# Performance work log

Hardware: AMD Instinct MI355X
Metric: run time of the kernel (lower is better)

Reference implementation:

```python
import jax, jax.numpy as jnp
import numpy as np

N = 512          # nodes per sample (num_nodes)
B = 8            # batch size (samples)
H = 64           # hidden_dim
SPARSITY = 0.1
K = int(SPARSITY * N * (N - 1))  # edges kept per sample (fixed, static)


def setup_inputs() -> dict:
    key = jax.random.key(0)
    ks = jax.random.split(key, 8)

    def lin(k, fi, fo):
        w = jax.random.normal(k, (fi, fo), jnp.float32) / np.sqrt(fi).astype(np.float32)
        b = jnp.zeros((fo,), jnp.float32)
        return w, b

    w_emb, b_emb = lin(ks[0], 1, H)
    w_proj, b_proj = lin(ks[1], H, H)
    w1, b1 = lin(ks[2], 2 * H, H)
    w2, b2 = lin(ks[3], H, H // 2)
    w3, b3 = lin(ks[4], H // 2, 1)
    x = jax.random.uniform(ks[5], (B * N, 1), jnp.float32)  # abundances >= 0
    batch = jnp.repeat(jnp.arange(B, dtype=jnp.int32), N)   # [B*N]
    return dict(x=x, w_emb=w_emb, b_emb=b_emb, w_proj=w_proj, b_proj=b_proj,
                w1=w1, b1=b1, w2=w2, b2=b2, w3=w3, b3=b3, batch=batch)


def reference(x, w_emb, b_emb, w_proj, b_proj, w1, b1, w2, b2, w3, b3, batch):
    # node embedding + projection (dropout is eval-mode no-op)
    emb = jax.nn.relu(x @ w_emb + b_emb) @ w_proj + b_proj     # [B*N, H]
    emb = emb.reshape(B, N, H)
    # first pairwise-MLP layer: cat([e_i, e_j]) @ w1 == e_i @ w1a + e_j @ w1b
    w1a, w1b = w1[:H], w1[H:]
    ai = emb @ w1a                                            # [B, N, H]
    aj = emb @ w1b                                            # [B, N, H]
    h1 = jax.nn.relu(ai[:, :, None, :] + aj[:, None, :, :] + b1)   # [B, N, N, H]
    h2 = jax.nn.relu(jnp.einsum('bijh,hk->bijk', h1, w2) + b2)     # [B, N, N, H/2]
    probs = jax.nn.sigmoid(jnp.einsum('bijk,ko->bij', h2, w3) + b3[0])  # [B, N, N]
    probs = 0.5 * (probs + jnp.swapaxes(probs, 1, 2))          # symmetrize
    probs = probs * (1.0 - jnp.eye(N, dtype=probs.dtype))      # mask diagonal
    flat = probs.reshape(B, N * N)
    _, idx = jax.lax.top_k(flat, K)                            # [B, K]
    idx = jnp.sort(idx, axis=-1)                               # row-major order (dense_to_sparse)
    vals = jnp.take_along_axis(flat, idx, axis=-1)             # [B, K]
    offsets = (jnp.arange(B) * N)[:, None]                     # node offset per sample
    rows = idx // N + offsets
    cols = idx % N + offsets
    edge_index = jnp.stack([rows.reshape(-1), cols.reshape(-1)], axis=0)  # [2, B*K]
    edge_weights = vals.reshape(-1)                            # [B*K]
    adj = jnp.zeros((B, N * N), flat.dtype).at[jnp.arange(B)[:, None], idx].set(vals)
    adj = adj.reshape(B, N, N)                                 # sparse adjacency per sample
    return edge_index, edge_weights, adj
```

## Files before the change

kernel.cpp:

```cpp
#include <hip/hip_runtime.h>

#define NV 512
#define BV 8
#define KSEL 26163
#define NNv (NV*NV)
#define BKv (BV*KSEL)
#define CAPB 32768
#define DELTA 1e-4f

typedef unsigned int u32;
typedef __attribute__((ext_vector_type(2))) float f32x2;
typedef __attribute__((ext_vector_type(4))) float f32x4;
typedef __attribute__((ext_vector_type(4))) u32 u32x4;
typedef __attribute__((ext_vector_type(8))) _Float16 f16x8;

__device__ __forceinline__ f32x2 pk_add(f32x2 a, f32x2 b) {
    f32x2 d; asm("v_pk_add_f32 %0, %1, %2" : "=v"(d) : "v"(a), "v"(b)); return d;
}
__device__ __forceinline__ f32x2 pk_fma(f32x2 a, f32x2 b, f32x2 c) {
    f32x2 d; asm("v_pk_fma_f32 %0, %1, %2, %3" : "=v"(d) : "v"(a), "v"(b), "v"(c)); return d;
}
__device__ __forceinline__ u32 pkrtz(float a, float b) {
    u32 d; asm("v_cvt_pkrtz_f16_f32 %0, %1, %2" : "=v"(d) : "v"(a), "v"(b)); return d;
}
__device__ __forceinline__ float fast_sigmoid(float z) {
    float e, p;
    asm("v_exp_f32 %0, %1" : "=v"(e) : "v"(-z * 1.44269504f));
    asm("v_rcp_f32 %0, %1" : "=v"(p) : "v"(1.f + e));
    return p;
}

__global__ void __launch_bounds__(256) k_embed(
    const float* __restrict__ x, const float* __restrict__ w_emb,
    const float* __restrict__ b_emb, const float* __restrict__ w_proj,
    const float* __restrict__ b_proj, const float* __restrict__ w1,
    const float* __restrict__ b1,
    float* __restrict__ ai, float* __restrict__ aj,
    float* __restrict__ ai256, float* __restrict__ ajb256) {
    __shared__ float sh[4][64];
    __shared__ float se[4][64];
    const int c = threadIdx.x;
    const int lr = threadIdx.y;
    const int row = blockIdx.x * 4 + lr;
    const float xv = x[row];
    sh[lr][c] = fmaxf(fmaf(xv, w_emb[c], b_emb[c]), 0.f);
    __syncthreads();
    float e = 0.f;
#pragma unroll
    for (int h = 0; h < 64; ++h) e = fmaf(sh[lr][h], w_proj[h * 64 + c], e);
    se[lr][c] = e + b_proj[c];
    __syncthreads();
    float a0 = 0.f, a1 = 0.f;
#pragma unroll
    for (int h = 0; h < 64; ++h) {
        const float ev = se[lr][h];
        a0 = fmaf(ev, w1[h * 64 + c], a0);
        a1 = fmaf(ev, w1[(64 + h) * 64 + c], a1);
    }
    ai[row * 64 + c] = a0;
    aj[row * 64 + c] = a1;
    ai256[row * 64 + c] = a0 * 256.0f;
    ajb256[row * 64 + c] = (a1 + b1[c]) * 256.0f;
}

__global__ void __launch_bounds__(256) k_pairs_sym(
    const float* __restrict__ ai256, const float* __restrict__ ajb256,
    const float* __restrict__ w2, const float* __restrict__ b2,
    const float* __restrict__ w3, const float* __restrict__ b3,
    float* __restrict__ probs, u32* __restrict__ hist8) {
    __shared__ float sI[2048];
    __shared__ float sJ[2048];
    __shared__ float sp1[32 * 33];
    __shared__ float sp2[32 * 33];
    __shared__ u32 lh[1024];
    const int tid = threadIdx.x;
    const int b = blockIdx.y;
    int remb = blockIdx.x, ta = 0;
    while (remb >= 16 - ta) { remb -= 16 - ta; ++ta; }
    const int tb = ta + remb;
    const int i0 = ta << 5, j0 = tb << 5;
    {
        const int r = tid >> 3, c8v = (tid & 7) << 3;
        const float* srcI = &ai256[(((b << 9) + i0 + r) << 6) + c8v];
        *(float4*)&sI[(r << 6) + c8v]     = *(const float4*)&srcI[0];
        *(float4*)&sI[(r << 6) + c8v + 4] = *(const float4*)&srcI[4];
        const float* srcJ = &ai256[(((b << 9) + j0 + r) << 6) + c8v];
        *(float4*)&sJ[(r << 6) + c8v]     = *(const float4*)&srcJ[0];
        *(float4*)&sJ[(r << 6) + c8v + 4] = *(const float4*)&srcJ[4];
        lh[tid] = 0; lh[256 + tid] = 0; lh[512 + tid] = 0; lh[768 + tid] = 0;
    }
    const int lane = tid & 63;
    const int lp = lane & 15, lg = lane >> 4;
    const int wave = tid >> 6;
    const int dir = wave >> 1, wc = wave & 1;
    const int colb = (wc << 4) + lp;
    const int colg = (dir ? i0 : j0) + colb;

    alignas(16) float ajr[2][8];
    {
        const float* base = &ajb256[(((b << 9) + colg) << 6) + (lg << 3)];
        *(float4*)&ajr[0][0] = *(const float4*)&base[0];
        *(float4*)&ajr[0][4] = *(const float4*)&base[4];
        *(float4*)&ajr[1][0] = *(const float4*)&base[32];
        *(float4*)&ajr[1][4] = *(const float4*)&base[36];
    }
    f16x8 Ah[2][2], Al[2][2];
#pragma unroll
    for (int kt = 0; kt < 2; ++kt)
#pragma unroll
        for (int ch = 0; ch < 2; ++ch)
#pragma unroll
            for (int e = 0; e < 8; ++e) {
                const float wv2 = w2[((ch << 5) + (lg << 3) + e) * 32 + (kt << 4) + lp];
                const _Float16 wh = (_Float16)wv2;
                Ah[kt][ch][e] = wh;
                Al[kt][ch][e] = (_Float16)((wv2 - (float)wh) * 2048.0f);
            }
    float b2f[2][4], w3f[2][4];
#pragma unroll
    for (int kt = 0; kt < 2; ++kt)
#pragma unroll
        for (int r = 0; r < 4; ++r) {
            b2f[kt][r] = b2[(kt << 4) + (lg << 2) + r] * 256.0f;
            w3f[kt][r] = w3[(kt << 4) + (lg << 2) + r] * 0.00390625f;
        }
    const float b3v = b3[0];
    __syncthreads();

    const float* __restrict__ sA = dir ? sJ : sI;
    float* __restrict__ spO = dir ? sp2 : sp1;
    const f32x2 CN1 = {-1.f, -1.f};

    for (int r = 0; r < 32; ++r) {
        alignas(16) float ar[2][8];
        *(float4*)&ar[0][0] = *(const float4*)&sA[(r << 6) + (lg << 3)];
        *(float4*)&ar[0][4] = *(const float4*)&sA[(r << 6) + (lg << 3) + 4];
        *(float4*)&ar[1][0] = *(const float4*)&sA[(r << 6) + 32 + (lg << 3)];
        *(float4*)&ar[1][4] = *(const float4*)&sA[(r << 6) + 32 + (lg << 3) + 4];
        alignas(16) u32 hw[2][4], lw[2][4];
#pragma unroll
        for (int c = 0; c < 2; ++c)
#pragma unroll
            for (int e2 = 0; e2 < 4; ++e2) {
                const f32x2 a2 = *(const f32x2*)&ar[c][e2 * 2];
                const f32x2 j2 = *(const f32x2*)&ajr[c][e2 * 2];
                f32x2 u2 = pk_add(a2, j2);
                u2[0] = fmaxf(u2[0], 0.f);
                u2[1] = fmaxf(u2[1], 0.f);
                hw[c][e2] = pkrtz(u2[0], u2[1]);
                f32x2 hif;
                hif[0] = __uint_as_float(__float_as_uint(u2[0]) & 0xFFFFE000u);
                hif[1] = __uint_as_float(__float_as_uint(u2[1]) & 0xFFFFE000u);
                const f32x2 lo = pk_fma(hif, CN1, u2);
                lw[c][e2] = pkrtz(lo[0], lo[1]);
            }
        const f16x8 Bh0 = __builtin_bit_cast(f16x8, *(u32x4*)&hw[0][0]);
        const f16x8 Bh1 = __builtin_bit_cast(f16x8, *(u32x4*)&hw[1][0]);
        const f16x8 Bl0 = __builtin_bit_cast(f16x8, *(u32x4*)&lw[0][0]);
        const f16x8 Bl1 = __builtin_bit_cast(f16x8, *(u32x4*)&lw[1][0]);
        f32x4 am0 = {0.f,0.f,0.f,0.f}, am1 = {0.f,0.f,0.f,0.f};
        f32x4 ac0 = {0.f,0.f,0.f,0.f}, ac1 = {0.f,0.f,0.f,0.f};
        am0 = __builtin_amdgcn_mfma_f32_16x16x32_f16(Ah[0][0], Bh0, am0, 0, 0, 0);
        am0 = __builtin_amdgcn_mfma_f32_16x16x32_f16(Ah[0][1], Bh1, am0, 0, 0, 0);
        am0 = __builtin_amdgcn_mfma_f32_16x16x32_f16(Ah[0][0], Bl0, am0, 0, 0, 0);
        am0 = __builtin_amdgcn_mfma_f32_16x16x32_f16(Ah[0][1], Bl1, am0, 0, 0, 0);
        ac0 = __builtin_amdgcn_mfma_f32_16x16x32_f16(Al[0][0], Bh0, ac0, 0, 0, 0);
        ac0 = __builtin_amdgcn_mfma_f32_16x16x32_f16(Al[0][1], Bh1, ac0, 0, 0, 0);
        am1 = __builtin_amdgcn_mfma_f32_16x16x32_f16(Ah[1][0], Bh0, am1, 0, 0, 0);
        am1 = __builtin_amdgcn_mfma_f32_16x16x32_f16(Ah[1][1], Bh1, am1, 0, 0, 0);
        am1 = __builtin_amdgcn_mfma_f32_16x16x32_f16(Ah[1][0], Bl0, am1, 0, 0, 0);
        am1 = __builtin_amdgcn_mfma_f32_16x16x32_f16(Ah[1][1], Bl1, am1, 0, 0, 0);
        ac1 = __builtin_amdgcn_mfma_f32_16x16x32_f16(Al[1][0], Bh0, ac1, 0, 0, 0);
        ac1 = __builtin_amdgcn_mfma_f32_16x16x32_f16(Al[1][1], Bh1, ac1, 0, 0, 0);
        float s = 0.f;
#pragma unroll
        for (int q = 0; q < 4; ++q) {
            const float amc = fmaf(ac0[q], 4.8828125e-4f, am0[q]);
            s = fmaf(fmaxf(amc + b2f[0][q], 0.f), w3f[0][q], s);
        }
#pragma unroll
        for (int q = 0; q < 4; ++q) {
            const float amc = fmaf(ac1[q], 4.8828125e-4f, am1[q]);
            s = fmaf(fmaxf(amc + b2f[1][q], 0.f), w3f[1][q], s);
        }
        s += __shfl_xor(s, 16);
        s += __shfl_xor(s, 32);
        const float p = fast_sigmoid(s + b3v);
        if (lane < 16) {
            if (dir == 0) spO[r * 33 + colb] = p;
            else          spO[colb * 33 + r] = p;
        }
    }
    __syncthreads();

    {
        const int pr = tid >> 3;
        const int pc = (tid & 7) << 2;
        const int rep = (tid & 3) << 8;
        const bool diag = (ta == tb);
        float4 vo;
        float vq[4];
#pragma unroll
        for (int q = 0; q < 4; ++q) {
            float v = 0.5f * (sp1[pr * 33 + pc + q] + sp2[pr * 33 + pc + q]);
            if (diag && pr == pc + q) v = 0.f;
            vq[q] = v;
            atomicAdd(&lh[rep + (__float_as_uint(v) >> 24)], diag ? 1u : 2u);
        }
        vo.x = vq[0]; vo.y = vq[1]; vo.z = vq[2]; vo.w = vq[3];
        *(float4*)&probs[(((b << 9) + i0 + pr) << 9) + j0 + pc] = vo;
        if (!diag) {
            float4 w4;
            w4.x = 0.5f * (sp1[(pc + 0) * 33 + pr] + sp2[(pc + 0) * 33 + pr]);
            w4.y = 0.5f * (sp1[(pc + 1) * 33 + pr] + sp2[(pc + 1) * 33 + pr]);
            w4.z = 0.5f * (sp1[(pc + 2) * 33 + pr] + sp2[(pc + 2) * 33 + pr]);
            w4.w = 0.5f * (sp1[(pc + 3) * 33 + pr] + sp2[(pc + 3) * 33 + pr]);
            *(float4*)&probs[(((b << 9) + j0 + pr) << 9) + i0 + pc] = w4;
        }
    }
    __syncthreads();
    const u32 sum = lh[tid] + lh[256 + tid] + lh[512 + tid] + lh[768 + tid];
    if (sum) atomicAdd(&hist8[b * 256 + tid], sum);
}

__global__ void __launch_bounds__(256) k_hist13(
    const float* __restrict__ probs, const u32* __restrict__ hist8,
    u32* __restrict__ hist13) {
    __shared__ u32 lh[8192];
    __shared__ u32 s8[256];
    __shared__ u32 selsh;
    const int t = threadIdx.x;
    const int b = blockIdx.y;
    for (int k = t; k < 8192; k += 256) lh[k] = 0u;
    s8[t] = hist8[b * 256 + t];
    __syncthreads();
    for (int off = 1; off < 256; off <<= 1) {
        const u32 v = (t + off < 256) ? s8[t + off] : 0u;
        __syncthreads();
        s8[t] += v;
        __syncthreads();
    }
    {
        const u32 above = (t < 255) ? s8[t + 1] : 0u;
        if (s8[t] >= (u32)KSEL && above < (u32)KSEL) selsh = (u32)t;
    }
    __syncthreads();
    const u32 sel = selsh;
    const float* Pb = probs + b * NNv;
    const int base = blockIdx.x * 4096 + t;
#pragma unroll
    for (int e = 0; e < 16; ++e) {
        const u32 key = __float_as_uint(Pb[base + e * 256]);
        if ((key >> 24) == sel) atomicAdd(&lh[(key >> 11) & 8191u], 1u);
    }
    __syncthreads();
    for (int k = t; k < 8192; k += 256) {
        const u32 v = lh[k];
        if (v) atomicAdd(&hist13[b * 8192 + k], v);
    }
}

__global__ void __launch_bounds__(256) k_sel13(
    const u32* __restrict__ hist8, const u32* __restrict__ hist13,
    float* __restrict__ thr) {
    __shared__ u32 s8[256];
    __shared__ u32 s[256];
    __shared__ u32 c8sh, remsh;
    const int b = blockIdx.x, t = threadIdx.x;
    s8[t] = hist8[b * 256 + t];
    __syncthreads();
    for (int off = 1; off < 256; off <<= 1) {
        const u32 v = (t + off < 256) ? s8[t + off] : 0u;
        __syncthreads();
        s8[t] += v;
        __syncthreads();
    }
    {
        const u32 above = (t < 255) ? s8[t + 1] : 0u;
        if (s8[t] >= (u32)KSEL && above < (u32)KSEL) {
            c8sh = (u32)t;
            remsh = (u32)KSEL - above;
        }
    }
    __syncthreads();
    const u32 c8 = c8sh, remv = remsh;
    const u32* H = hist13 + b * 8192;
    u32 sum = 0;
    for (int k = 0; k < 32; ++k) sum += H[t * 32 + k];
    s[t] = sum;
    __syncthreads();
    for (int off = 1; off < 256; off <<= 1) {
        const u32 v = (t + off < 256) ? s[t + off] : 0u;
        __syncthreads();
        s[t] += v;
        __syncthreads();
    }
    const u32 above = (t < 255) ? s[t + 1] : 0u;
    if (s[t] >= remv && above < remv) {
        u32 cum = above;
        int c = 31;
        for (; c >= 0; --c) {
            cum += H[t * 32 + c];
            if (cum >= remv) break;
        }
        const u32 p21 = (c8 << 13) | (u32)(t * 32 + c);
        thr[b]     = __uint_as_float(p21 << 11) - 2.f * DELTA;
        thr[8 + b] = __uint_as_float((p21 + 1u) << 11) + 2.f * DELTA;
    }
}

__device__ __forceinline__ float exact_p(const float* __restrict__ rai,
                                         const float* __restrict__ raj,
                                         const float* __restrict__ s_w2,
                                         const float* __restrict__ s_b1,
                                         const float* __restrict__ s_b2,
                                         const float* __restrict__ s_w3,
                                         float b3v) {
    float acc[32];
#pragma unroll
    for (int k = 0; k < 32; ++k) acc[k] = 0.f;
#pragma unroll 1
    for (int h0 = 0; h0 < 64; h0 += 16) {
        float A[16], J[16];
#pragma unroll
        for (int q = 0; q < 4; ++q) {
            *(float4*)&A[q * 4] = *(const float4*)&rai[h0 + q * 4];
            *(float4*)&J[q * 4] = *(const float4*)&raj[h0 + q * 4];
        }
#pragma unroll
        for (int hh = 0; hh < 16; ++hh) {
            const float tv = fmaxf((A[hh] + J[hh]) + s_b1[h0 + hh], 0.f);
#pragma unroll
            for (int k = 0; k < 32; ++k) acc[k] = fmaf(tv, s_w2[(h0 + hh) * 32 + k], acc[k]);
        }
    }
    float d = 0.f;
#pragma unroll
    for (int k = 0; k < 32; ++k) d = fmaf(fmaxf(acc[k] + s_b2[k], 0.f), s_w3[k], d);
    return 1.f / (1.f + expf(-(d + b3v)));
}

__global__ void __launch_bounds__(256) k_band(
    const float* __restrict__ P, const float* __restrict__ thr,
    const float* __restrict__ ai, const float* __restrict__ aj,
    const float* __restrict__ b1, const float* __restrict__ w2,
    const float* __restrict__ b2, const float* __restrict__ w3,
    const float* __restrict__ b3,
    u32* __restrict__ C_in, u32* __restrict__ bandCnt,
    u32* __restrict__ bandIdx, float* __restrict__ bandVal,
    u32* __restrict__ bgt) {
    __shared__ float s_w2[2048];
    __shared__ float s_b1[64], s_b2[32], s_w3[32];
    __shared__ u32 lidx[2048];
    __shared__ u32 lcnt, lhi, gbase;
    const int b = blockIdx.y, blk = blockIdx.x, t = threadIdx.x;
    {
        const int o = t * 8;
        *(float4*)&s_w2[o]     = *(const float4*)&w2[o];
        *(float4*)&s_w2[o + 4] = *(const float4*)&w2[o + 4];
        if (t < 64) s_b1[t] = b1[t];
        if (t < 32) { s_b2[t] = b2[t]; s_w3[t] = w3[t]; }
        if (t == 0) { lcnt = 0u; lhi = 0u; }
    }
    __syncthreads();
    const float Tlo = thr[b], Thi = thr[8 + b];
    const int fi0 = blk * 1024 + t * 4;
    const float4 v = *(const float4*)&P[b * NNv + fi0];
    const float vv[4] = {v.x, v.y, v.z, v.w};
    u32 hc = 0;
#pragma unroll
    for (int q = 0; q < 4; ++q) {
        const float xq = vv[q];
        if (xq > Thi) ++hc;
        else if (xq >= Tlo) {
            const u32 p = atomicAdd(&lcnt, 1u);
            if (p < 2048u) lidx[p] = (u32)(fi0 + q);
        }
    }
    if (hc) atomicAdd(&lhi, hc);
    __syncthreads();
    if (t == 0) {
        bgt[b * 256 + blk] = lhi;
        if (lhi) atomicAdd(&C_in[b], lhi);
        gbase = lcnt ? atomicAdd(&bandCnt[b], lcnt) : 0u;
    }
    __syncthreads();
    const u32 ln = min(lcnt, 2048u);
    const float b3v = b3[0];
    for (u32 p = t; p < ln; p += 256) {
        const u32 g = gbase + p;
        if (g < (u32)CAPB) {
            const u32 idx = lidx[p];
            const int i = (int)(idx >> 9), j = (int)(idx & 511u);
            const float* ri  = &ai[(((b << 9) + i)) << 6];
            const float* rj  = &aj[(((b << 9) + j)) << 6];
            const float* rj2 = &ai[(((b << 9) + j)) << 6];
            const float* ri2 = &aj[(((b << 9) + i)) << 6];
            const float p1 = exact_p(ri, rj, s_w2, s_b1, s_b2, s_w3, b3v);
            const float p2 = exact_p(rj2, ri2, s_w2, s_b1, s_b2, s_w3, b3v);
            bandIdx[b * CAPB + g] = idx;
            bandVal[b * CAPB + g] = 0.5f * (p1 + p2);
        }
    }
}

__global__ void __launch_bounds__(256) k_band_select(
    const u32* __restrict__ bandCnt, const u32* __restrict__ C_in,
    const u32* __restrict__ bandIdx, const float* __restrict__ bandVal,
    u32* __restrict__ bitmap, const u32* __restrict__ bgt,
    u32* __restrict__ goff) {
    __shared__ u32 red[256];
    __shared__ u32 lsel[256];
    __shared__ u32 tie[8192];
    __shared__ u32 tieCnt;
    const int b = blockIdx.x, t = threadIdx.x;
    const u32 nb = min(bandCnt[b], (u32)CAPB);
    const u32 Kp = (u32)KSEL - C_in[b];
    const u32* vb = (const u32*)(bandVal + b * CAPB);
    const u32* ib = bandIdx + b * CAPB;
    u32* bm = bitmap + b * 8192;
    lsel[t] = 0u;
    u32 mn = 0xFFFFFFFFu, mx = 0u;
    for (u32 k = t; k < nb; k += 256) { const u32 v = vb[k]; mn = min(mn, v); mx = max(mx, v); }
    red[t] = mn; __syncthreads();
    for (int s = 128; s > 0; s >>= 1) { if (t < s) red[t] = min(red[t], red[t + s]); __syncthreads(); }
    const u32 glo = red[0]; __syncthreads();
    red[t] = mx; __syncthreads();
    for (int s = 128; s > 0; s >>= 1) { if (t < s) red[t] = max(red[t], red[t + s]); __syncthreads(); }
    const u32 ghi = red[0]; __syncthreads();
    u32 lo = glo, hi = ghi;
    while (lo < hi) {
        const u32 mid = lo + ((hi - lo) >> 1);
        u32 c = 0;
        for (u32 k = t; k < nb; k += 256) c += (vb[k] > mid);
        red[t] = c; __syncthreads();
        for (int s = 128; s > 0; s >>= 1) { if (t < s) red[t] += red[t + s]; __syncthreads(); }
        const u32 tot = red[0]; __syncthreads();
        if (tot >= Kp) lo = mid + 1; else hi = mid;
    }
    const u32 Tx = lo;
    if (t == 0) tieCnt = 0u;
    __syncthreads();
    u32 c = 0;
    for (u32 k = t; k < nb; k += 256) {
        const u32 v = vb[k];
        if (v > Tx) {
            ++c;
            const u32 idx = ib[k];
            atomicOr(&bm[idx >> 5], 1u << (idx & 31u));
            atomicAdd(&lsel[idx >> 10], 1u);
        } else if (v == Tx) {
            const u32 p = atomicAdd(&tieCnt, 1u);
            if (p < 8192u) tie[p] = ib[k];
        }
    }
    red[t] = c; __syncthreads();
    for (int s = 128; s > 0; s >>= 1) { if (t < s) red[t] += red[t + s]; __syncthreads(); }
    const u32 Ap = red[0]; __syncthreads();
    const u32 Rp = Kp - Ap;
    const u32 E = min(tieCnt, 8192u);
    for (u32 k = t; k < E; k += 256) {
        const u32 my = tie[k];
        u32 r = 0;
        for (u32 m = 0; m < E; ++m) r += (tie[m] < my);
        if (r < Rp) {
            atomicOr(&bm[my >> 5], 1u << (my & 31u));
            atomicAdd(&lsel[my >> 10], 1u);
        }
    }
    __syncthreads();
    const u32 g = bgt[b * 256 + t] + lsel[t];
    red[t] = g;
    __syncthreads();
    for (int off = 1; off < 256; off <<= 1) {
        const u32 a = (t >= off) ? red[t - off] : 0u;
        __syncthreads();
        red[t] += a;
        __syncthreads();
    }
    goff[b * 256 + t] = red[t] - g;
}

__global__ void k_write(const float* __restrict__ P, const float* __restrict__ thr,
                        const u32* __restrict__ bitmap, const u32* __restrict__ goff,
                        float* __restrict__ out) {
    __shared__ u32 sg[256];
    const int b = blockIdx.y, blk = blockIdx.x, t = threadIdx.x;
    const float Thi = thr[8 + b];
    const int pbase = b * NNv;
    const int fi0 = blk * 1024 + t * 4;
    const float4 v = *(const float4*)&P[pbase + fi0];
    const float vv[4] = {v.x, v.y, v.z, v.w};
    const u32 w = bitmap[b * 8192 + (fi0 >> 5)];
    const u32 sh = (u32)(fi0 & 31);
    bool sel[4];
    u32 cnt = 0;
#pragma unroll
    for (int q = 0; q < 4; ++q) {
        sel[q] = (vv[q] > Thi) || ((w >> (sh + q)) & 1u);
        cnt += sel[q];
    }
    sg[t] = cnt;
    __syncthreads();
    for (int off = 1; off < 256; off <<= 1) {
        const u32 a = (t >= off) ? sg[t - off] : 0u;
        __syncthreads();
        sg[t] += a;
        __syncthreads();
    }
    u32 pos = goff[b * 256 + blk] + sg[t] - cnt;
#pragma unroll
    for (int q = 0; q < 4; ++q) {
        if (sel[q]) {
            if (pos < (u32)KSEL) {
                const int g = b * KSEL + (int)pos;
                const int fi = fi0 + q;
                const int row = fi >> 9, col = fi & 511;
                out[g]           = (float)(row + (b << 9));
                out[BKv + g]     = (float)(col + (b << 9));
                out[2 * BKv + g] = vv[q];
                out[3 * BKv + pbase + fi] = vv[q];
            }
            ++pos;
        }
    }
}

extern "C" void kernel_launch(void* const* d_in, const int* in_sizes, int n_in,
                              void* d_out, int out_size, void* d_ws, size_t ws_size,
                              hipStream_t stream) {
    const float* x      = (const float*)d_in[0];
    const float* w_emb  = (const float*)d_in[1];
    const float* b_emb  = (const float*)d_in[2];
    const float* w_proj = (const float*)d_in[3];
    const float* b_proj = (const float*)d_in[4];
    const float* w1     = (const float*)d_in[5];
    const float* b1     = (const float*)d_in[6];
    const float* w2     = (const float*)d_in[7];
    const float* b2     = (const float*)d_in[8];
    const float* w3     = (const float*)d_in[9];
    const float* b3     = (const float*)d_in[10];
    (void)in_sizes; (void)n_in; (void)ws_size;

    char* ws = (char*)d_ws;
    float* ai      = (float*)(ws);
    float* aj      = (float*)(ws + 1048576);
    float* ai256   = (float*)(ws + 2097152);
    float* ajb256  = (float*)(ws + 3145728);
    float* probs   = (float*)(ws + 4194304);
    u32*   bandIdx = (u32*)  (ws + 12582912);
    float* bandVal = (float*)(ws + 13631488);
    const size_t SOFF = 14680064;
    u32*   hist8   = (u32*)  (ws + SOFF);
    u32*   hist13  = (u32*)  (ws + SOFF + 8192);
    float* thr     = (float*)(ws + SOFF + 270336);
    u32*   C_in    = (u32*)  (ws + SOFF + 270400);
    u32*   bandCnt = (u32*)  (ws + SOFF + 270432);
    u32*   bitmap  = (u32*)  (ws + SOFF + 270464);
    u32*   bgt     = (u32*)  (ws + SOFF + 532608);
    u32*   goff    = (u32*)  (ws + SOFF + 540800);

    float* out = (float*)d_out;

    hipMemsetAsync(d_out, 0, (size_t)out_size * sizeof(float), stream);
    hipMemsetAsync(ws + SOFF, 0, 532608, stream);

    k_embed<<<1024, dim3(64, 4, 1), 0, stream>>>(x, w_emb, b_emb, w_proj, b_proj,
                                                 w1, b1, ai, aj, ai256, ajb256);
    k_pairs_sym<<<dim3(136, 8), 256, 0, stream>>>(ai256, ajb256, w2, b2, w3, b3,
                                                  probs, hist8);
    k_hist13<<<dim3(64, 8), 256, 0, stream>>>(probs, hist8, hist13);
    k_sel13<<<8, 256, 0, stream>>>(hist8, hist13, thr);
    k_band<<<dim3(256, 8), 256, 0, stream>>>(probs, thr, ai, aj, b1, w2, b2, w3, b3,
                                             C_in, bandCnt, bandIdx, bandVal, bgt);
    k_band_select<<<8, 256, 0, stream>>>(bandCnt, C_in, bandIdx, bandVal,
                                         bitmap, bgt, goff);
    k_write<<<dim3(256, 8), 256, 0, stream>>>(probs, thr, bitmap, goff, out);
}
```

Measured before the change: 198.5 us.

## Split band exact recompute into separate load-balanced kernel; vectorize hist13 loads

```diff
diff --git a/kernel.cpp b/kernel.cpp
--- a/kernel.cpp
+++ b/kernel.cpp
@@ -247,11 +247,16 @@
     __syncthreads();
     const u32 sel = selsh;
     const float* Pb = probs + b * NNv;
-    const int base = blockIdx.x * 4096 + t;
-#pragma unroll
-    for (int e = 0; e < 16; ++e) {
-        const u32 key = __float_as_uint(Pb[base + e * 256]);
-        if ((key >> 24) == sel) atomicAdd(&lh[(key >> 11) & 8191u], 1u);
+    const int base = blockIdx.x * 4096 + t * 4;
+#pragma unroll
+    for (int e = 0; e < 4; ++e) {
+        const float4 v4 = *(const float4*)&Pb[base + e * 1024];
+        const float vv[4] = {v4.x, v4.y, v4.z, v4.w};
+#pragma unroll
+        for (int q = 0; q < 4; ++q) {
+            const u32 key = __float_as_uint(vv[q]);
+            if ((key >> 24) == sel) atomicAdd(&lh[(key >> 11) & 8191u], 1u);
+        }
     }
     __syncthreads();
     for (int k = t; k < 8192; k += 256) {
@@ -309,6 +314,44 @@
     }
 }
 
+__global__ void __launch_bounds__(256) k_band(
+    const float* __restrict__ P, const float* __restrict__ thr,
+    u32* __restrict__ C_in, u32* __restrict__ bandCnt, u32* __restrict__ bandIdx,
+    u32* __restrict__ bgt) {
+    __shared__ u32 lidx[2048];
+    __shared__ u32 lcnt, lhi, gbase;
+    const int b = blockIdx.y, blk = blockIdx.x, t = threadIdx.x;
+    if (t == 0) { lcnt = 0u; lhi = 0u; }
+    __syncthreads();
+    const float Tlo = thr[b], Thi = thr[8 + b];
+    const int fi0 = blk * 1024 + t * 4;
+    const float4 v = *(const float4*)&P[b * NNv + fi0];
+    const float vv[4] = {v.x, v.y, v.z, v.w};
+    u32 hc = 0;
+#pragma unroll
+    for (int q = 0; q < 4; ++q) {
+        const float xq = vv[q];
+        if (xq > Thi) ++hc;
+        else if (xq >= Tlo) {
+            const u32 p = atomicAdd(&lcnt, 1u);
+            if (p < 2048u) lidx[p] = (u32)(fi0 + q);
+        }
+    }
+    if (hc) atomicAdd(&lhi, hc);
+    __syncthreads();
+    const u32 ln = min(lcnt, 2048u);
+    if (t == 0) {
+        bgt[b * 256 + blk] = lhi;
+        if (lhi) atomicAdd(&C_in[b], lhi);
+        gbase = ln ? atomicAdd(&bandCnt[b], ln) : 0u;
+    }
+    __syncthreads();
+    for (u32 p = t; p < ln; p += 256) {
+        const u32 g = gbase + p;
+        if (g < (u32)CAPB) bandIdx[b * CAPB + g] = lidx[p];
+    }
+}
+
 __device__ __forceinline__ float exact_p(const float* __restrict__ rai,
                                          const float* __restrict__ raj,
                                          const float* __restrict__ s_w2,
@@ -340,67 +383,35 @@
     return 1.f / (1.f + expf(-(d + b3v)));
 }
 
-__global__ void __launch_bounds__(256) k_band(
-    const float* __restrict__ P, const float* __restrict__ thr,
+__global__ void __launch_bounds__(256) k_band_exact(
     const float* __restrict__ ai, const float* __restrict__ aj,
     const float* __restrict__ b1, const float* __restrict__ w2,
     const float* __restrict__ b2, const float* __restrict__ w3,
-    const float* __restrict__ b3,
-    u32* __restrict__ C_in, u32* __restrict__ bandCnt,
-    u32* __restrict__ bandIdx, float* __restrict__ bandVal,
-    u32* __restrict__ bgt) {
+    const float* __restrict__ b3, const u32* __restrict__ bandCnt,
+    const u32* __restrict__ bandIdx, float* __restrict__ bandVal) {
     __shared__ float s_w2[2048];
     __shared__ float s_b1[64], s_b2[32], s_w3[32];
-    __shared__ u32 lidx[2048];
-    __shared__ u32 lcnt, lhi, gbase;
-    const int b = blockIdx.y, blk = blockIdx.x, t = threadIdx.x;
+    const int b = blockIdx.y, t = threadIdx.x;
     {
         const int o = t * 8;
         *(float4*)&s_w2[o]     = *(const float4*)&w2[o];
         *(float4*)&s_w2[o + 4] = *(const float4*)&w2[o + 4];
         if (t < 64) s_b1[t] = b1[t];
         if (t < 32) { s_b2[t] = b2[t]; s_w3[t] = w3[t]; }
-        if (t == 0) { lcnt = 0u; lhi = 0u; }
-    }
-    __syncthreads();
-    const float Tlo = thr[b], Thi = thr[8 + b];
-    const int fi0 = blk * 1024 + t * 4;
-    const float4 v = *(const float4*)&P[b * NNv + fi0];
-    const float vv[4] = {v.x, v.y, v.z, v.w};
-    u32 hc = 0;
-#pragma unroll
-    for (int q = 0; q < 4; ++q) {
-        const float xq = vv[q];
-        if (xq > Thi) ++hc;
-        else if (xq >= Tlo) {
-            const u32 p = atomicAdd(&lcnt, 1u);
-            if (p < 2048u) lidx[p] = (u32)(fi0 + q);
-        }
-    }
-    if (hc) atomicAdd(&lhi, hc);
-    __syncthreads();
-    if (t == 0) {
-        bgt[b * 256 + blk] = lhi;
-        if (lhi) atomicAdd(&C_in[b], lhi);
-        gbase = lcnt ? atomicAdd(&bandCnt[b], lcnt) : 0u;
-    }
-    __syncthreads();
-    const u32 ln = min(lcnt, 2048u);
+    }
+    __syncthreads();
+    const u32 nb = min(bandCnt[b], (u32)CAPB);
     const float b3v = b3[0];
-    for (u32 p = t; p < ln; p += 256) {
-        const u32 g = gbase + p;
-        if (g < (u32)CAPB) {
-            const u32 idx = lidx[p];
-            const int i = (int)(idx >> 9), j = (int)(idx & 511u);
-            const float* ri  = &ai[(((b << 9) + i)) << 6];
-            const float* rj  = &aj[(((b << 9) + j)) << 6];
-            const float* rj2 = &ai[(((b << 9) + j)) << 6];
-            const float* ri2 = &aj[(((b << 9) + i)) << 6];
-            const float p1 = exact_p(ri, rj, s_w2, s_b1, s_b2, s_w3, b3v);
-            const float p2 = exact_p(rj2, ri2, s_w2, s_b1, s_b2, s_w3, b3v);
-            bandIdx[b * CAPB + g] = idx;
-            bandVal[b * CAPB + g] = 0.5f * (p1 + p2);
-        }
+    for (u32 e = blockIdx.x * 256 + t; e < nb; e += 8192) {
+        const u32 idx = bandIdx[b * CAPB + e];
+        const int i = (int)(idx >> 9), j = (int)(idx & 511u);
+        const float* ri  = &ai[(((b << 9) + i)) << 6];
+        const float* rj  = &aj[(((b << 9) + j)) << 6];
+        const float* rj2 = &ai[(((b << 9) + j)) << 6];
+        const float* ri2 = &aj[(((b << 9) + i)) << 6];
+        const float p1 = exact_p(ri, rj, s_w2, s_b1, s_b2, s_w3, b3v);
+        const float p2 = exact_p(rj2, ri2, s_w2, s_b1, s_b2, s_w3, b3v);
+        bandVal[b * CAPB + e] = 0.5f * (p1 + p2);
     }
 }
 
@@ -571,8 +582,9 @@
                                                   probs, hist8);
     k_hist13<<<dim3(64, 8), 256, 0, stream>>>(probs, hist8, hist13);
     k_sel13<<<8, 256, 0, stream>>>(hist8, hist13, thr);
-    k_band<<<dim3(256, 8), 256, 0, stream>>>(probs, thr, ai, aj, b1, w2, b2, w3, b3,
-                                             C_in, bandCnt, bandIdx, bandVal, bgt);
+    k_band<<<dim3(256, 8), 256, 0, stream>>>(probs, thr, C_in, bandCnt, bandIdx, bgt);
+    k_band_exact<<<dim3(32, 8), 256, 0, stream>>>(ai, aj, b1, w2, b2, w3, b3,
+                                                  bandCnt, bandIdx, bandVal);
     k_band_select<<<8, 256, 0, stream>>>(bandCnt, C_in, bandIdx, bandVal,
                                          bitmap, bgt, goff);
     k_write<<<dim3(256, 8), 256, 0, stream>>>(probs, thr, bitmap, goff, out);
```

Measured after the change: 196.2 us. No clear change (-1.2%).
